# Kernel tuning notes

Hardware: AMD Instinct MI355X
Metric: run time of the kernel (lower is better)

## Reference

```python
import jax, jax.numpy as jnp
import numpy as np

EPSILON = 1e-06
N_TOKENS = 65536
WIDTH_IN = 1024
WIDTH_OUT = 1024
NUM_HEAD = 16
DIM_HEAD = 64


def setup_inputs() -> dict:
    key = jax.random.key(0)
    k_x, k_b, k_lin, k_ker = jax.random.split(key, 4)
    x = jax.random.normal(k_x, (N_TOKENS, WIDTH_IN), dtype=jnp.float32)
    norm_bias = jax.random.normal(k_b, (N_TOKENS, NUM_HEAD, DIM_HEAD), dtype=jnp.float32)
    # LinearLayer: std = 1/sqrt(width_in), shape (width_in, num_head*dim_head)
    w_lin = jax.random.normal(k_lin, (WIDTH_IN, NUM_HEAD * DIM_HEAD), dtype=jnp.float32) / np.sqrt(WIDTH_IN)
    # Grouped kernel: (num_head, dim_head, width_out // num_head), scaled 1/sqrt(dim_head)
    kernel = jax.random.normal(k_ker, (NUM_HEAD, DIM_HEAD, WIDTH_OUT // NUM_HEAD), dtype=jnp.float32) / np.sqrt(DIM_HEAD)
    return {"x": x, "norm_bias": norm_bias, "w_lin": w_lin, "kernel": kernel}


def reference(x, norm_bias, w_lin, kernel):
    # Dense projection, bias-free
    xx = x @ w_lin                                   # [N, H*D]
    xx = xx.reshape(*x.shape[:-1], NUM_HEAD, DIM_HEAD)  # [N, H, D]
    # Per-head RMSNorm
    xx = xx / jnp.sqrt(jnp.mean(jnp.square(xx), axis=-1, keepdims=True) + EPSILON)
    # Optional norm-bias blend
    xx = (xx + norm_bias.reshape(xx.shape)) / 2 ** 0.5
    # Per-head grouped matmul
    xx = jnp.einsum('nhd,hdf->nhf', xx, kernel)      # [N, H, F]
    return xx.reshape(*x.shape[:-1], -1)             # [N, H*F]
```

## Files before the change

### kernel.cpp

```cpp
#include <hip/hip_runtime.h>


typedef __attribute__((ext_vector_type(8))) __bf16 bf16x8;
typedef __attribute__((ext_vector_type(4))) float f32x4;
typedef __attribute__((ext_vector_type(8))) unsigned short ushort8;

__device__ __forceinline__ unsigned short bfbits(float f) {
  return __builtin_bit_cast(unsigned short, (__bf16)f);
}
__device__ __forceinline__ f32x4 mfma_bf16(bf16x8 a, bf16x8 b, f32x4 c) {
  return __builtin_amdgcn_mfma_f32_16x16x32_bf16(a, b, c, 0, 0, 0);
}
__device__ __forceinline__ void gl_lds16(const void* g, void* l) {
  __builtin_amdgcn_global_load_lds(
      (const __attribute__((address_space(1))) unsigned int*)g,
      (__attribute__((address_space(3))) unsigned int*)l, 16, 0, 0);
}

__global__ void prep_w2(const float* __restrict__ w, unsigned short* __restrict__ wb) {
  const int t = blockIdx.x, ct = blockIdx.y, col = threadIdx.x;
  #pragma unroll
  for (int kc = 0; kc < 4; ++kc) {
    ushort8 v;
    #pragma unroll
    for (int j = 0; j < 8; ++j)
      v[j] = bfbits(w[(size_t)(t * 32 + kc * 8 + j) * 1024 + ct * 128 + col]);
    *reinterpret_cast<ushort8*>(wb + (((size_t)(ct * 32 + t) * 4 + kc) * 128 + col) * 8) = v;
  }
}

__global__ void transpose_k(const float* __restrict__ kin, unsigned short* __restrict__ kt) {
  __shared__ float tile[64][65];
  const int h = blockIdx.x;
  const int t = threadIdx.x;
  #pragma unroll
  for (int i = 0; i < 16; ++i) {
    int idx = i * 256 + t;
    tile[idx >> 6][idx & 63] = kin[(size_t)h * 4096 + idx];
  }
  __syncthreads();
  #pragma unroll
  for (int i = 0; i < 16; ++i) {
    int idx = i * 256 + t;
    kt[(size_t)h * 4096 + idx] = bfbits(tile[idx & 63][idx >> 6]);
  }
}

__global__ __launch_bounds__(256, 3)
void fused_main(const float* __restrict__ x,
                const float* __restrict__ nbias,
                const unsigned short* __restrict__ wb,
                const unsigned short* __restrict__ ktg,
                float* __restrict__ out)
{
  __shared__ __align__(16) unsigned char smem[32768];
  const int tid = threadIdx.x;
  const int wv = tid >> 6, lane = tid & 63, l15 = lane & 15, lg = lane >> 4;
  const int wr = wv >> 1, wc = wv & 1;
  const int bid = blockIdx.x;
  const int gx = bid & 7, slot = bid >> 3;
  const int v = gx * 512 + slot;
  const int rt = v >> 3, ct = v & 7;
  const size_t row0 = (size_t)rt * 128;

  const int sr = tid >> 1, sh = tid & 1;
  const float* agp = x + (row0 + sr) * 1024 + sh * 16;
  const unsigned char* wsrc =
      reinterpret_cast<const unsigned char*>(wb) + (size_t)ct * 262144;

  const int aoff = lg * 2048 + (wr * 64 + l15) * 16;
  const int boff = lg * 2048 + (wc * 64 + l15) * 16;

  f32x4 acc[4][4];
  const f32x4 z4 = {0.f, 0.f, 0.f, 0.f};
  #pragma unroll
  for (int mi = 0; mi < 4; ++mi)
    #pragma unroll
    for (int ni = 0; ni < 4; ++ni) acc[mi][ni] = z4;

  f32x4 arg[2][4];

  auto stageB = [&](int t, int bsel) {
    unsigned char* Bb = smem + 16384 + (bsel << 13);
    const unsigned char* bs = wsrc + (size_t)t * 8192;
    gl_lds16(bs + tid * 16,        Bb + tid * 16);
    gl_lds16(bs + 4096 + tid * 16, Bb + 4096 + tid * 16);
  };
  auto loadA = [&](int t, f32x4* dst) {
    const float* p = agp + t * 32;
    #pragma unroll
    for (int j = 0; j < 4; ++j) dst[j] = *reinterpret_cast<const f32x4*>(p + j * 4);
  };
  auto cvtwrA = [&](const f32x4* src, int bsel) {
    unsigned char* Ab = smem + (bsel << 13);
    ushort8 v0, v1;
    #pragma unroll
    for (int j = 0; j < 4; ++j) { v0[j] = bfbits(src[0][j]); v0[4 + j] = bfbits(src[1][j]); }
    #pragma unroll
    for (int j = 0; j < 4; ++j) { v1[j] = bfbits(src[2][j]); v1[4 + j] = bfbits(src[3][j]); }
    *reinterpret_cast<ushort8*>(Ab + (2 * sh) * 2048 + sr * 16)     = v0;
    *reinterpret_cast<ushort8*>(Ab + (2 * sh + 1) * 2048 + sr * 16) = v1;
  };
  auto compute = [&](int csel) {
    const unsigned char* Ab = smem + (csel << 13);
    const unsigned char* Bb = smem + 16384 + (csel << 13);
    bf16x8 af[4], bq[4];
    #pragma unroll
    for (int mi = 0; mi < 4; ++mi)
      af[mi] = *reinterpret_cast<const bf16x8*>(Ab + aoff + mi * 256);
    #pragma unroll
    for (int ni = 0; ni < 4; ++ni)
      bq[ni] = *reinterpret_cast<const bf16x8*>(Bb + boff + ni * 256);
    __builtin_amdgcn_s_setprio(1);
    #pragma unroll
    for (int mi = 0; mi < 4; ++mi)
      #pragma unroll
      for (int ni = 0; ni < 4; ++ni)
        acc[mi][ni] = mfma_bf16(af[mi], bq[ni], acc[mi][ni]);
    __builtin_amdgcn_s_setprio(0);
  };

  stageB(0, 0);
  loadA(0, arg[0]);
  loadA(1, arg[1]);
  __builtin_amdgcn_sched_barrier(0);
  cvtwrA(arg[0], 0);
  asm volatile("s_waitcnt lgkmcnt(0)" ::: "memory");
  __builtin_amdgcn_sched_barrier(0);
  __builtin_amdgcn_s_barrier();
  __builtin_amdgcn_sched_barrier(0);

  #pragma unroll
  for (int t = 0; t < 32; ++t) {
    const int c = t & 1, n = c ^ 1;
    if (t + 1 < 32) { stageB(t + 1, n); __builtin_amdgcn_sched_barrier(0); }
    if (t + 2 < 32) { loadA(t + 2, arg[c]); __builtin_amdgcn_sched_barrier(0); }

    compute(c);
    if (t + 1 < 32) cvtwrA(arg[n], n);

    if (t + 1 < 32) {
      asm volatile("s_waitcnt lgkmcnt(0)" ::: "memory");
      if (t + 2 < 32) asm volatile("s_waitcnt vmcnt(4)" ::: "memory");
      else            asm volatile("s_waitcnt vmcnt(0)" ::: "memory");
      __builtin_amdgcn_sched_barrier(0);
      __builtin_amdgcn_s_barrier();
      __builtin_amdgcn_sched_barrier(0);
    }
  }
  __builtin_amdgcn_sched_barrier(0);
  __syncthreads();

  const int h = ct * 2 + wc;
  unsigned short* yw = reinterpret_cast<unsigned short*>(smem) + wv * 4096;
  const float* bb = nbias + (row0 + wr * 64) * 1024 + (size_t)h * 64 + l15;

  #pragma unroll
  for (int mi = 0; mi < 4; ++mi) {
    float ss[4];
    #pragma unroll
    for (int r = 0; r < 4; ++r) {
      float p = 0.f;
      #pragma unroll
      for (int ni = 0; ni < 4; ++ni) { const float q = acc[mi][ni][r]; p += q * q; }
      ss[r] = p;
    }
    #pragma unroll
    for (int s = 1; s < 16; s <<= 1)
      #pragma unroll
      for (int r = 0; r < 4; ++r) ss[r] += __shfl_xor(ss[r], s, 64);
    #pragma unroll
    for (int r = 0; r < 4; ++r) {
      const float rs = rsqrtf(ss[r] * 0.015625f + 1e-6f);
      const int rl = mi * 16 + lg * 4 + r;
      const float* bp = bb + (size_t)rl * 1024;
      #pragma unroll
      for (int ni = 0; ni < 4; ++ni) {
        const float y = (acc[mi][ni][r] * rs + bp[ni * 16]) * 0.70710678118654752f;
        yw[rl * 64 + ((ni * 16 + l15) ^ ((rl & 7) << 3))] = bfbits(y);
      }
    }
  }

  const unsigned short* ktp = ktg + (size_t)h * 4096;
  bf16x8 b2[4][2];
  #pragma unroll
  for (int ff = 0; ff < 4; ++ff)
    #pragma unroll
    for (int ks = 0; ks < 2; ++ks)
      b2[ff][ks] = *reinterpret_cast<const bf16x8*>(ktp + (ff * 16 + l15) * 64 + ks * 32 + lg * 8);

  #pragma unroll
  for (int m2 = 0; m2 < 4; ++m2) {
    f32x4 a2[4] = {z4, z4, z4, z4};
    const int row = m2 * 16 + l15;
    #pragma unroll
    for (int ks = 0; ks < 2; ++ks) {
      bf16x8 a = *reinterpret_cast<const bf16x8*>(
          yw + row * 64 + ((ks * 32 + lg * 8) ^ ((row & 7) << 3)));
      #pragma unroll
      for (int ff = 0; ff < 4; ++ff) a2[ff] = mfma_bf16(a, b2[ff][ks], a2[ff]);
    }
    float* ob = out + (row0 + wr * 64 + m2 * 16 + lg * 4) * 1024 + ct * 128 + wc * 64 + l15;
    #pragma unroll
    for (int ff = 0; ff < 4; ++ff)
      #pragma unroll
      for (int r = 0; r < 4; ++r)
        ob[(size_t)r * 1024 + ff * 16] = a2[ff][r];
  }
}

extern "C" void kernel_launch(void* const* d_in, const int* in_sizes, int n_in,
                              void* d_out, int out_size, void* d_ws, size_t ws_size,
                              hipStream_t stream) {
  const float* x  = (const float*)d_in[0];
  const float* nb = (const float*)d_in[1];
  const float* wl = (const float*)d_in[2];
  const float* kr = (const float*)d_in[3];
  float* out = (float*)d_out;

  unsigned short* wbp = (unsigned short*)d_ws;
  unsigned short* ktp = wbp + 1048576;

  hipLaunchKernelGGL(prep_w2, dim3(32, 8), dim3(128), 0, stream, wl, wbp);
  hipLaunchKernelGGL(transpose_k, dim3(16), dim3(256), 0, stream, kr, ktp);
  hipLaunchKernelGGL(fused_main, dim3(4096), dim3(256), 0, stream, x, nb, wbp, ktp, out);
}
```

Baseline: 330.5 us.

## Pre-convert x to bf16 and stream A tiles straight into LDS

Adds a separate kernel that converts x from fp32 to bf16 in workspace. The main GEMM can then load A tiles with global_load_lds into a swizzled LDS layout, instead of doing register loads, converting and writing to LDS. The hand-tuned waitcnt/sched_barrier pipeline is replaced by a simple double-buffered loop with __syncthreads. Occupancy is raised to 4 blocks per CU. The trade-off is an extra full pass over x: a 256MB read plus a 128MB write. The simpler synchronisation may also reduce overlap between loads and MFMA.

Result: faster. 321.4 us (-2.7%).

```diff
diff --git a/kernel.cpp b/kernel.cpp
--- a/kernel.cpp
+++ b/kernel.cpp
@@ -17,6 +17,19 @@
       (__attribute__((address_space(3))) unsigned int*)l, 16, 0, 0);
 }
 
+__global__ void cvt_x(const float* __restrict__ x, unsigned short* __restrict__ xb, int n8) {
+  int i = blockIdx.x * blockDim.x + threadIdx.x;
+  const int stride = gridDim.x * blockDim.x;
+  for (; i < n8; i += stride) {
+    f32x4 a = *reinterpret_cast<const f32x4*>(x + (size_t)i * 8);
+    f32x4 b = *reinterpret_cast<const f32x4*>(x + (size_t)i * 8 + 4);
+    ushort8 v;
+    v[0] = bfbits(a[0]); v[1] = bfbits(a[1]); v[2] = bfbits(a[2]); v[3] = bfbits(a[3]);
+    v[4] = bfbits(b[0]); v[5] = bfbits(b[1]); v[6] = bfbits(b[2]); v[7] = bfbits(b[3]);
+    *reinterpret_cast<ushort8*>(xb + (size_t)i * 8) = v;
+  }
+}
+
 __global__ void prep_w2(const float* __restrict__ w, unsigned short* __restrict__ wb) {
   const int t = blockIdx.x, ct = blockIdx.y, col = threadIdx.x;
   #pragma unroll
@@ -46,8 +59,8 @@
   }
 }
 
-__global__ __launch_bounds__(256, 3)
-void fused_main(const float* __restrict__ x,
+__global__ __launch_bounds__(256, 4)
+void fused_main(const unsigned short* __restrict__ xb,
                 const float* __restrict__ nbias,
                 const unsigned short* __restrict__ wb,
                 const unsigned short* __restrict__ ktg,
@@ -63,13 +76,17 @@
   const int rt = v >> 3, ct = v & 7;
   const size_t row0 = (size_t)rt * 128;
 
-  const int sr = tid >> 1, sh = tid & 1;
-  const float* agp = x + (row0 + sr) * 1024 + sh * 16;
-  const unsigned char* wsrc =
-      reinterpret_cast<const unsigned char*>(wb) + (size_t)ct * 262144;
-
-  const int aoff = lg * 2048 + (wr * 64 + l15) * 16;
-  const int boff = lg * 2048 + (wc * 64 + l15) * 16;
+  const unsigned char* xrow = reinterpret_cast<const unsigned char*>(xb) + row0 * 2048;
+  const unsigned char* wsrc = reinterpret_cast<const unsigned char*>(wb) + (size_t)ct * 262144;
+
+  const int c0 = tid,       r0_ = c0 >> 2, s0_ = c0 & 3;
+  const int c1 = 256 + tid, r1_ = c1 >> 2;
+  const unsigned char* asrc0 = xrow + r0_ * 2048 + ((s0_ ^ ((r0_ >> 1) & 3)) << 4);
+  const unsigned char* asrc1 = xrow + r1_ * 2048 + ((s0_ ^ ((r1_ >> 1) & 3)) << 4);
+
+  const int swz_a = (l15 >> 1) & 3;
+  const int abase = (wr * 64 + l15) * 64 + ((lg ^ swz_a) << 4);
+  const int bbase = lg * 2048 + (wc * 64 + l15) * 16;
 
   f32x4 acc[4][4];
   const f32x4 z4 = {0.f, 0.f, 0.f, 0.f};
@@ -78,39 +95,27 @@
     #pragma unroll
     for (int ni = 0; ni < 4; ++ni) acc[mi][ni] = z4;
 
-  f32x4 arg[2][4];
-
+  auto stageA = [&](int t, int bsel) {
+    unsigned char* Ab = smem + (bsel << 13);
+    gl_lds16(asrc0 + (size_t)t * 64, Ab + tid * 16);
+    gl_lds16(asrc1 + (size_t)t * 64, Ab + 4096 + tid * 16);
+  };
   auto stageB = [&](int t, int bsel) {
     unsigned char* Bb = smem + 16384 + (bsel << 13);
     const unsigned char* bs = wsrc + (size_t)t * 8192;
     gl_lds16(bs + tid * 16,        Bb + tid * 16);
     gl_lds16(bs + 4096 + tid * 16, Bb + 4096 + tid * 16);
   };
-  auto loadA = [&](int t, f32x4* dst) {
-    const float* p = agp + t * 32;
-    #pragma unroll
-    for (int j = 0; j < 4; ++j) dst[j] = *reinterpret_cast<const f32x4*>(p + j * 4);
-  };
-  auto cvtwrA = [&](const f32x4* src, int bsel) {
-    unsigned char* Ab = smem + (bsel << 13);
-    ushort8 v0, v1;
-    #pragma unroll
-    for (int j = 0; j < 4; ++j) { v0[j] = bfbits(src[0][j]); v0[4 + j] = bfbits(src[1][j]); }
-    #pragma unroll
-    for (int j = 0; j < 4; ++j) { v1[j] = bfbits(src[2][j]); v1[4 + j] = bfbits(src[3][j]); }
-    *reinterpret_cast<ushort8*>(Ab + (2 * sh) * 2048 + sr * 16)     = v0;
-    *reinterpret_cast<ushort8*>(Ab + (2 * sh + 1) * 2048 + sr * 16) = v1;
-  };
   auto compute = [&](int csel) {
     const unsigned char* Ab = smem + (csel << 13);
     const unsigned char* Bb = smem + 16384 + (csel << 13);
     bf16x8 af[4], bq[4];
     #pragma unroll
     for (int mi = 0; mi < 4; ++mi)
-      af[mi] = *reinterpret_cast<const bf16x8*>(Ab + aoff + mi * 256);
+      af[mi] = *reinterpret_cast<const bf16x8*>(Ab + abase + mi * 1024);
     #pragma unroll
     for (int ni = 0; ni < 4; ++ni)
-      bq[ni] = *reinterpret_cast<const bf16x8*>(Bb + boff + ni * 256);
+      bq[ni] = *reinterpret_cast<const bf16x8*>(Bb + bbase + ni * 256);
     __builtin_amdgcn_s_setprio(1);
     #pragma unroll
     for (int mi = 0; mi < 4; ++mi)
@@ -120,35 +125,15 @@
     __builtin_amdgcn_s_setprio(0);
   };
 
+  stageA(0, 0);
   stageB(0, 0);
-  loadA(0, arg[0]);
-  loadA(1, arg[1]);
-  __builtin_amdgcn_sched_barrier(0);
-  cvtwrA(arg[0], 0);
-  asm volatile("s_waitcnt lgkmcnt(0)" ::: "memory");
-  __builtin_amdgcn_sched_barrier(0);
-  __builtin_amdgcn_s_barrier();
-  __builtin_amdgcn_sched_barrier(0);
-
-  #pragma unroll
+
   for (int t = 0; t < 32; ++t) {
-    const int c = t & 1, n = c ^ 1;
-    if (t + 1 < 32) { stageB(t + 1, n); __builtin_amdgcn_sched_barrier(0); }
-    if (t + 2 < 32) { loadA(t + 2, arg[c]); __builtin_amdgcn_sched_barrier(0); }
-
-    compute(c);
-    if (t + 1 < 32) cvtwrA(arg[n], n);
-
-    if (t + 1 < 32) {
-      asm volatile("s_waitcnt lgkmcnt(0)" ::: "memory");
-      if (t + 2 < 32) asm volatile("s_waitcnt vmcnt(4)" ::: "memory");
-      else            asm volatile("s_waitcnt vmcnt(0)" ::: "memory");
-      __builtin_amdgcn_sched_barrier(0);
-      __builtin_amdgcn_s_barrier();
-      __builtin_amdgcn_sched_barrier(0);
-    }
-  }
-  __builtin_amdgcn_sched_barrier(0);
+    __syncthreads();
+    const int cur = t & 1, nxt = cur ^ 1;
+    if (t + 1 < 32) { stageA(t + 1, nxt); stageB(t + 1, nxt); }
+    compute(cur);
+  }
   __syncthreads();
 
   const int h = ct * 2 + wc;
@@ -221,8 +206,10 @@
 
   unsigned short* wbp = (unsigned short*)d_ws;
   unsigned short* ktp = wbp + 1048576;
+  unsigned short* xbp = (unsigned short*)((char*)d_ws + 2228224);
 
   hipLaunchKernelGGL(prep_w2, dim3(32, 8), dim3(128), 0, stream, wl, wbp);
   hipLaunchKernelGGL(transpose_k, dim3(16), dim3(256), 0, stream, kr, ktp);
-  hipLaunchKernelGGL(fused_main, dim3(4096), dim3(256), 0, stream, x, nb, wbp, ktp, out);
-}
+  hipLaunchKernelGGL(cvt_x, dim3(2048), dim3(256), 0, stream, x, xbp, 65536 * 128);
+  hipLaunchKernelGGL(fused_main, dim3(4096), dim3(256), 0, stream, xbp, nb, wbp, ktp, out);
+}
```
